# Performance work log

Hardware: AMD Instinct MI355X
Metric: run time of the kernel (lower is better)

Reference implementation:

```python
import jax, jax.numpy as jnp
import numpy as np

NDIM = 1024
NHEAD = 16
HEAD_DIM = NDIM // NHEAD


def setup_inputs() -> dict:
    key = jax.random.key(0)
    ks = jax.random.split(key, 12)
    B, L, C = 2, 2048, NDIM
    s = 0.02
    return {
        "q": jax.random.normal(ks[0], (B, L, C), jnp.float32),
        "k": jax.random.normal(ks[1], (B, L, C), jnp.float32),
        "v": jax.random.normal(ks[2], (B, L, C), jnp.float32),
        "Wq": jax.random.normal(ks[3], (C, C), jnp.float32) * s,
        "bq": jax.random.normal(ks[4], (C,), jnp.float32) * s,
        "Wk": jax.random.normal(ks[5], (C, C), jnp.float32) * s,
        "bk": jax.random.normal(ks[6], (C,), jnp.float32) * s,
        "Wv": jax.random.normal(ks[7], (C, C), jnp.float32) * s,
        "bv": jax.random.normal(ks[8], (C,), jnp.float32) * s,
        "Wo": jax.random.normal(ks[9], (C, C), jnp.float32) * s,
        "bo": jax.random.normal(ks[10], (C,), jnp.float32) * s,
    }


def reference(q, k, v, Wq, bq, Wk, bk, Wv, bv, Wo, bo):
    B, Lq, C = q.shape
    H, D = NHEAD, HEAD_DIM
    # projections, then split heads: (B, H, L, D)
    qh = (q @ Wq + bq).reshape(B, Lq, H, D).transpose(0, 2, 1, 3)
    kh = (k @ Wk + bk).reshape(B, k.shape[1], H, D).transpose(0, 2, 1, 3)
    vh = (v @ Wv + bv).reshape(B, v.shape[1], H, D).transpose(0, 2, 1, 3)
    scale = 1.0 / jnp.sqrt(jnp.asarray(D, qh.dtype))
    att = jnp.einsum("bhqd,bhkd->bhqk", qh, kh) * scale  # (B,H,Lq,Lk)
    att = jax.nn.softmax(att, axis=-1)  # dropout p=0.0 -> identity
    y = jnp.einsum("bhqk,bhkd->bhqd", att, vh)
    y = y.transpose(0, 2, 1, 3).reshape(B, Lq, C)
    return y @ Wo + bo
```

## Files before the change

kernel.cpp:

```cpp
#include <hip/hip_runtime.h>
#include <math.h>

#define BATCH 2
#define SEQ   2048
#define CDIM  1024
#define NHEAD 16
#define HDIM  64
#define TOKS  (BATCH * SEQ)

typedef __bf16 bf16x8 __attribute__((ext_vector_type(8)));
typedef float  f32x4  __attribute__((ext_vector_type(4)));

#define MFMA16(a, b, c) __builtin_amdgcn_mfma_f32_16x16x32_bf16(a, b, c, 0, 0, 0)

#define QSCALE 0.1803368801111204f

__device__ __forceinline__ void gload_lds16(const __bf16* g, __bf16* l) {
    __builtin_amdgcn_global_load_lds(
        (const __attribute__((address_space(1))) unsigned int*)g,
        (__attribute__((address_space(3))) unsigned int*)l, 16, 0, 0);
}

__global__ __launch_bounds__(256) void prep_kernel(
    const float* __restrict__ q, const float* __restrict__ k, const float* __restrict__ v,
    __bf16* __restrict__ qo, __bf16* __restrict__ ko, __bf16* __restrict__ vo,
    const float* __restrict__ W0, const float* __restrict__ W1,
    const float* __restrict__ W2, const float* __restrict__ W3,
    __bf16* __restrict__ T0, __bf16* __restrict__ T1,
    __bf16* __restrict__ T2, __bf16* __restrict__ T3)
{
    __shared__ __bf16 Ts[64][72];
    const int bx = blockIdx.x;
    const int tid = threadIdx.x;

    if (bx < 6144) {
        const int t = bx >> 11;
        const size_t i = ((size_t)(bx & 2047) * 256 + tid) * 8;
        const float* s = t == 0 ? q : (t == 1 ? k : v);
        __bf16* d = t == 0 ? qo : (t == 1 ? ko : vo);
        const float4 x = *(const float4*)&s[i];
        const float4 y = *(const float4*)&s[i + 4];
        bf16x8 o;
        o[0] = (__bf16)x.x; o[1] = (__bf16)x.y; o[2] = (__bf16)x.z; o[3] = (__bf16)x.w;
        o[4] = (__bf16)y.x; o[5] = (__bf16)y.y; o[6] = (__bf16)y.z; o[7] = (__bf16)y.w;
        *(bf16x8*)&d[i] = o;
        return;
    }

    const int t  = bx - 6144;
    const int z  = t >> 8;
    const int ry = (t & 255) >> 4;
    const int rx = t & 15;
    const float* W = z == 0 ? W0 : z == 1 ? W1 : z == 2 ? W2 : W3;
    __bf16* T = z == 0 ? T0 : z == 1 ? T1 : z == 2 ? T2 : T3;
    const int rb = ry * 64, cb = rx * 64;
    const int r = tid >> 4;
    const int c4 = (tid & 15) * 4;
#pragma unroll
    for (int p = 0; p < 4; p++) {
        const int rr = p * 16 + r;
        const float4 w4 = *(const float4*)&W[(size_t)(rb + rr) * CDIM + cb + c4];
        Ts[c4 + 0][rr] = (__bf16)w4.x;
        Ts[c4 + 1][rr] = (__bf16)w4.y;
        Ts[c4 + 2][rr] = (__bf16)w4.z;
        Ts[c4 + 3][rr] = (__bf16)w4.w;
    }
    __syncthreads();
    const int n = tid >> 2;
    const int k16 = (tid & 3) * 16;
    *(bf16x8*)&T[(size_t)(cb + n) * CDIM + rb + k16]     = *(const bf16x8*)&Ts[n][k16];
    *(bf16x8*)&T[(size_t)(cb + n) * CDIM + rb + k16 + 8] = *(const bf16x8*)&Ts[n][k16 + 8];
}

__global__ __launch_bounds__(256) void qkv_gemm_kernel(
    const __bf16* __restrict__ qb, const __bf16* __restrict__ kb,
    const __bf16* __restrict__ vb,
    const __bf16* __restrict__ Wqt, const __bf16* __restrict__ Wkt,
    const __bf16* __restrict__ Wvt,
    const float* __restrict__ bq, const float* __restrict__ bk,
    const float* __restrict__ bv,
    __bf16* __restrict__ Qh, __bf16* __restrict__ Kh, __bf16* __restrict__ Vht)
{
    __shared__ __bf16 As[128 * 32];
    __shared__ __bf16 Bs[128 * 32];

    const int z = blockIdx.z;
    const __bf16* A    = z == 0 ? qb : z == 1 ? kb : Wvt;
    const __bf16* Bt   = z == 0 ? Wqt : z == 1 ? Wkt : vb;
    const float*  bias = z == 0 ? bq : z == 1 ? bk : bv;

    const int tid  = threadIdx.x;
    const int w    = tid >> 6;
    const int lane = tid & 63;
    const int quad = lane >> 4;
    const int c    = lane & 15;
    const int wm   = w >> 1;
    const int wn   = w & 1;
    const int rowBase = (z == 2 ? blockIdx.x : blockIdx.y) * 128;
    const int colBase = (z == 2 ? blockIdx.y : blockIdx.x) * 128;

    const int sr = lane >> 2;
    const int sk = (lane & 3) * 8;

    f32x4 acc[4][4];
#pragma unroll
    for (int i = 0; i < 4; i++)
#pragma unroll
        for (int j = 0; j < 4; j++) acc[i][j] = (f32x4){0, 0, 0, 0};

    for (int k0 = 0; k0 < CDIM; k0 += 32) {
#pragma unroll
        for (int j = 0; j < 2; j++) {
            const int r0 = (w * 2 + j) * 16;
            gload_lds16(A  + (size_t)(rowBase + r0 + sr) * CDIM + k0 + sk, &As[r0 * 32]);
            gload_lds16(Bt + (size_t)(colBase + r0 + sr) * CDIM + k0 + sk, &Bs[r0 * 32]);
        }
        __syncthreads();

        bf16x8 af[4], bf[4];
#pragma unroll
        for (int i = 0; i < 4; i++) {
            af[i] = *(const bf16x8*)&As[(wm * 64 + i * 16 + c) * 32 + quad * 8];
            bf[i] = *(const bf16x8*)&Bs[(wn * 64 + i * 16 + c) * 32 + quad * 8];
        }
#pragma unroll
        for (int mi = 0; mi < 4; mi++)
#pragma unroll
            for (int ni = 0; ni < 4; ni++)
                acc[mi][ni] = MFMA16(af[mi], bf[ni], acc[mi][ni]);
        __syncthreads();
    }

#pragma unroll
    for (int mi = 0; mi < 4; mi++) {
#pragma unroll
        for (int ni = 0; ni < 4; ni++) {
            const int col = colBase + wn * 64 + ni * 16 + c;
#pragma unroll
            for (int r = 0; r < 4; r++) {
                const int row = rowBase + wm * 64 + mi * 16 + quad * 4 + r;
                const float val = acc[mi][ni][r];
                if (z == 2) {
                    Vht[(size_t)row * TOKS + col] = (__bf16)(val + bias[row]);
                } else {
                    const int b = row >> 11, l = row & 2047;
                    const int h = col >> 6,  d = col & 63;
                    const float s = (z == 0) ? QSCALE : 1.0f;
                    __bf16* outp = (z == 0) ? Qh : Kh;
                    outp[((((size_t)b * NHEAD + h) * SEQ) + l) * HDIM + d] =
                        (__bf16)((val + bias[col]) * s);
                }
            }
        }
    }
}

__global__ __launch_bounds__(256) void out_gemm_kernel(
    const __bf16* __restrict__ A, const __bf16* __restrict__ Bt,
    const float* __restrict__ bias, float* __restrict__ out)
{
    __shared__ __bf16 As[128 * 32];
    __shared__ __bf16 Bs[128 * 32];

    const int tid  = threadIdx.x;
    const int w    = tid >> 6;
    const int lane = tid & 63;
    const int quad = lane >> 4;
    const int c    = lane & 15;
    const int wm   = w >> 1;
    const int wn   = w & 1;
    const int rowBase = blockIdx.y * 128;
    const int colBase = blockIdx.x * 128;
    const int sr = lane >> 2;
    const int sk = (lane & 3) * 8;

    f32x4 acc[4][4];
#pragma unroll
    for (int i = 0; i < 4; i++)
#pragma unroll
        for (int j = 0; j < 4; j++) acc[i][j] = (f32x4){0, 0, 0, 0};

    for (int k0 = 0; k0 < CDIM; k0 += 32) {
#pragma unroll
        for (int j = 0; j < 2; j++) {
            const int r0 = (w * 2 + j) * 16;
            gload_lds16(A  + (size_t)(rowBase + r0 + sr) * CDIM + k0 + sk, &As[r0 * 32]);
            gload_lds16(Bt + (size_t)(colBase + r0 + sr) * CDIM + k0 + sk, &Bs[r0 * 32]);
        }
        __syncthreads();

        bf16x8 af[4], bf[4];
#pragma unroll
        for (int i = 0; i < 4; i++) {
            af[i] = *(const bf16x8*)&As[(wm * 64 + i * 16 + c) * 32 + quad * 8];
            bf[i] = *(const bf16x8*)&Bs[(wn * 64 + i * 16 + c) * 32 + quad * 8];
        }
#pragma unroll
        for (int mi = 0; mi < 4; mi++)
#pragma unroll
            for (int ni = 0; ni < 4; ni++)
                acc[mi][ni] = MFMA16(af[mi], bf[ni], acc[mi][ni]);
        __syncthreads();
    }

#pragma unroll
    for (int mi = 0; mi < 4; mi++) {
#pragma unroll
        for (int ni = 0; ni < 4; ni++) {
            const int col = colBase + wn * 64 + ni * 16 + c;
#pragma unroll
            for (int r = 0; r < 4; r++) {
                const int row = rowBase + wm * 64 + mi * 16 + quad * 4 + r;
                out[(size_t)row * CDIM + col] = acc[mi][ni][r] + bias[col];
            }
        }
    }
}

__global__ __launch_bounds__(256) void attn_mfma_kernel(
    const __bf16* __restrict__ Qh, const __bf16* __restrict__ Kh,
    const __bf16* __restrict__ Vht, __bf16* __restrict__ Y)
{
    __shared__ __align__(16) __bf16 Ks[32][72];
    __shared__ __align__(16) __bf16 Vt[64][48];
    __shared__ __align__(16) __bf16 Pf[4][32][48];

    const int tid  = threadIdx.x;
    const int w    = tid >> 6;
    const int lane = tid & 63;
    const int quad = lane >> 4;
    const int c    = lane & 15;
    const int bh   = blockIdx.x;
    const int b    = bh >> 4;
    const int h    = bh & 15;
    const int qbase = blockIdx.y * 128 + w * 32;

    const __bf16* Qg = Qh + (size_t)bh * SEQ * HDIM;
    const __bf16* Kg = Kh + (size_t)bh * SEQ * HDIM;
    const __bf16* Vg = Vht + (size_t)(h * HDIM) * TOKS + (size_t)b * SEQ;

    bf16x8 qf[2][2];
#pragma unroll
    for (int g = 0; g < 2; g++) {
        qf[g][0] = *(const bf16x8*)&Qg[(size_t)(qbase + g * 16 + c) * HDIM + quad * 8];
        qf[g][1] = *(const bf16x8*)&Qg[(size_t)(qbase + g * 16 + c) * HDIM + 32 + quad * 8];
    }

    bf16x8 ones;
#pragma unroll
    for (int j = 0; j < 8; j++) ones[j] = (__bf16)1.0f;

    f32x4 O[2][4];
    f32x4 L[2];
#pragma unroll
    for (int g = 0; g < 2; g++) {
        L[g] = (f32x4){0, 0, 0, 0};
#pragma unroll
        for (int i = 0; i < 4; i++) O[g][i] = (f32x4){0, 0, 0, 0};
    }

    const int skey = tid >> 3, sc8 = (tid & 7) * 8;
    const int sd   = tid >> 2, sk8 = (tid & 3) * 8;

    for (int t0 = 0; t0 < SEQ; t0 += 32) {
        __syncthreads();
        *(bf16x8*)&Ks[skey][sc8] = *(const bf16x8*)&Kg[(size_t)(t0 + skey) * HDIM + sc8];
        *(bf16x8*)&Vt[sd][sk8]   = *(const bf16x8*)&Vg[(size_t)sd * TOKS + t0 + sk8];
        __syncthreads();

        const bf16x8 k00 = *(const bf16x8*)&Ks[c][quad * 8];
        const bf16x8 k01 = *(const bf16x8*)&Ks[c][32 + quad * 8];
        const bf16x8 k10 = *(const bf16x8*)&Ks[16 + c][quad * 8];
        const bf16x8 k11 = *(const bf16x8*)&Ks[16 + c][32 + quad * 8];

#pragma unroll
        for (int g = 0; g < 2; g++) {
            f32x4 s0 = {0, 0, 0, 0}, s1 = {0, 0, 0, 0};
            s0 = MFMA16(qf[g][0], k00, s0);
            s0 = MFMA16(qf[g][1], k01, s0);
            s1 = MFMA16(qf[g][0], k10, s1);
            s1 = MFMA16(qf[g][1], k11, s1);
#pragma unroll
            for (int r = 0; r < 4; r++) {
                Pf[w][g * 16 + quad * 4 + r][c]      = (__bf16)__builtin_amdgcn_exp2f(s0[r]);
                Pf[w][g * 16 + quad * 4 + r][16 + c] = (__bf16)__builtin_amdgcn_exp2f(s1[r]);
            }
        }

        const bf16x8 v0 = *(const bf16x8*)&Vt[c][quad * 8];
        const bf16x8 v1 = *(const bf16x8*)&Vt[16 + c][quad * 8];
        const bf16x8 v2 = *(const bf16x8*)&Vt[32 + c][quad * 8];
        const bf16x8 v3 = *(const bf16x8*)&Vt[48 + c][quad * 8];

#pragma unroll
        for (int g = 0; g < 2; g++) {
            const bf16x8 pf = *(const bf16x8*)&Pf[w][g * 16 + c][quad * 8];
            L[g]    = MFMA16(pf, ones, L[g]);
            O[g][0] = MFMA16(pf, v0, O[g][0]);
            O[g][1] = MFMA16(pf, v1, O[g][1]);
            O[g][2] = MFMA16(pf, v2, O[g][2]);
            O[g][3] = MFMA16(pf, v3, O[g][3]);
        }
    }

    __bf16* Yb = Y + (size_t)b * SEQ * CDIM;
#pragma unroll
    for (int g = 0; g < 2; g++) {
#pragma unroll
        for (int r = 0; r < 4; r++) {
            const float inv = 1.0f / L[g][r];
            const int l = qbase + g * 16 + quad * 4 + r;
            __bf16* yp = Yb + (size_t)l * CDIM + h * HDIM + c;
            yp[0]  = (__bf16)(O[g][0][r] * inv);
            yp[16] = (__bf16)(O[g][1][r] * inv);
            yp[32] = (__bf16)(O[g][2][r] * inv);
            yp[48] = (__bf16)(O[g][3][r] * inv);
        }
    }
}


extern "C" void kernel_launch(void* const* d_in, const int* in_sizes, int n_in,
                              void* d_out, int out_size, void* d_ws, size_t ws_size,
                              hipStream_t stream)
{
    const float* q  = (const float*)d_in[0];
    const float* k  = (const float*)d_in[1];
    const float* v  = (const float*)d_in[2];
    const float* Wq = (const float*)d_in[3];
    const float* bq = (const float*)d_in[4];
    const float* Wk = (const float*)d_in[5];
    const float* bk = (const float*)d_in[6];
    const float* Wv = (const float*)d_in[7];
    const float* bv = (const float*)d_in[8];
    const float* Wo = (const float*)d_in[9];
    const float* bo = (const float*)d_in[10];
    float* out = (float*)d_out;

    const size_t MAT = (size_t)TOKS * CDIM;
    const size_t WN  = (size_t)CDIM * CDIM;

    __bf16* p   = (__bf16*)d_ws;
    __bf16* qb  = p; p += MAT;
    __bf16* kb  = p; p += MAT;
    __bf16* vb  = p; p += MAT;
    __bf16* Wqt = p; p += WN;
    __bf16* Wkt = p; p += WN;
    __bf16* Wvt = p; p += WN;
    __bf16* Wot = p; p += WN;
    __bf16* Qh  = p; p += MAT;
    __bf16* Kh  = p; p += MAT;
    __bf16* Vht = p; p += MAT;
    __bf16* Yb  = qb;

    const dim3 blk(256);

    prep_kernel<<<dim3(6144 + 1024), blk, 0, stream>>>(
        q, k, v, qb, kb, vb, Wq, Wk, Wv, Wo, Wqt, Wkt, Wvt, Wot);

    qkv_gemm_kernel<<<dim3(8, 32, 3), blk, 0, stream>>>(
        qb, kb, vb, Wqt, Wkt, Wvt, bq, bk, bv, Qh, Kh, Vht);

    attn_mfma_kernel<<<dim3(BATCH * NHEAD, SEQ / 128), blk, 0, stream>>>(Qh, Kh, Vht, Yb);

    out_gemm_kernel<<<dim3(8, 32), blk, 0, stream>>>(Yb, Wot, bo, out);
}
```

Baseline: 248.0 us.

## Rewrite attention as single-wave register-pipelined kernel; permute V layout; narrow output tiles

The attention kernel now runs one wave per block over 64 queries. K and V fragments are loaded straight from global memory into double-buffered registers, replacing the LDS staging and block barriers. V is stored with a permuted column order so the P fragments can be written to LDS as packed bf16 pairs. The output GEMM tile drops from 128x128 to 128x64 to launch more blocks. The cost is more register pressure and uncoalesced global loads in attention, plus less data reuse per block in the output GEMM.

After: 262.7 us. 1.06x slower.

```diff
diff --git a/kernel.cpp b/kernel.cpp
--- a/kernel.cpp
+++ b/kernel.cpp
@@ -9,6 +9,7 @@
 #define TOKS  (BATCH * SEQ)
 
 typedef __bf16 bf16x8 __attribute__((ext_vector_type(8)));
+typedef __bf16 bf16x2 __attribute__((ext_vector_type(2)));
 typedef float  f32x4  __attribute__((ext_vector_type(4)));
 
 #define MFMA16(a, b, c) __builtin_amdgcn_mfma_f32_16x16x32_bf16(a, b, c, 0, 0, 0)
@@ -141,7 +142,8 @@
                 const int row = rowBase + wm * 64 + mi * 16 + quad * 4 + r;
                 const float val = acc[mi][ni][r];
                 if (z == 2) {
-                    Vht[(size_t)row * TOKS + col] = (__bf16)(val + bias[row]);
+                    const int col2 = (col & ~31) | (((col & 15) << 1) | ((col >> 4) & 1));
+                    Vht[(size_t)row * TOKS + col2] = (__bf16)(val + bias[row]);
                 } else {
                     const int b = row >> 11, l = row & 2047;
                     const int h = col >> 6,  d = col & 63;
@@ -160,7 +162,7 @@
     const float* __restrict__ bias, float* __restrict__ out)
 {
     __shared__ __bf16 As[128 * 32];
-    __shared__ __bf16 Bs[128 * 32];
+    __shared__ __bf16 Bs[64 * 32];
 
     const int tid  = threadIdx.x;
     const int w    = tid >> 6;
@@ -170,35 +172,36 @@
     const int wm   = w >> 1;
     const int wn   = w & 1;
     const int rowBase = blockIdx.y * 128;
-    const int colBase = blockIdx.x * 128;
+    const int colBase = blockIdx.x * 64;
     const int sr = lane >> 2;
     const int sk = (lane & 3) * 8;
 
-    f32x4 acc[4][4];
+    f32x4 acc[4][2];
 #pragma unroll
     for (int i = 0; i < 4; i++)
 #pragma unroll
-        for (int j = 0; j < 4; j++) acc[i][j] = (f32x4){0, 0, 0, 0};
+        for (int j = 0; j < 2; j++) acc[i][j] = (f32x4){0, 0, 0, 0};
 
     for (int k0 = 0; k0 < CDIM; k0 += 32) {
 #pragma unroll
         for (int j = 0; j < 2; j++) {
             const int r0 = (w * 2 + j) * 16;
-            gload_lds16(A  + (size_t)(rowBase + r0 + sr) * CDIM + k0 + sk, &As[r0 * 32]);
-            gload_lds16(Bt + (size_t)(colBase + r0 + sr) * CDIM + k0 + sk, &Bs[r0 * 32]);
-        }
+            gload_lds16(A + (size_t)(rowBase + r0 + sr) * CDIM + k0 + sk, &As[r0 * 32]);
+        }
+        gload_lds16(Bt + (size_t)(colBase + w * 16 + sr) * CDIM + k0 + sk, &Bs[w * 16 * 32]);
         __syncthreads();
 
-        bf16x8 af[4], bf[4];
-#pragma unroll
-        for (int i = 0; i < 4; i++) {
+        bf16x8 af[4], bf[2];
+#pragma unroll
+        for (int i = 0; i < 4; i++)
             af[i] = *(const bf16x8*)&As[(wm * 64 + i * 16 + c) * 32 + quad * 8];
-            bf[i] = *(const bf16x8*)&Bs[(wn * 64 + i * 16 + c) * 32 + quad * 8];
-        }
+#pragma unroll
+        for (int i = 0; i < 2; i++)
+            bf[i] = *(const bf16x8*)&Bs[(wn * 32 + i * 16 + c) * 32 + quad * 8];
 #pragma unroll
         for (int mi = 0; mi < 4; mi++)
 #pragma unroll
-            for (int ni = 0; ni < 4; ni++)
+            for (int ni = 0; ni < 2; ni++)
                 acc[mi][ni] = MFMA16(af[mi], bf[ni], acc[mi][ni]);
         __syncthreads();
     }
@@ -206,8 +209,8 @@
 #pragma unroll
     for (int mi = 0; mi < 4; mi++) {
 #pragma unroll
-        for (int ni = 0; ni < 4; ni++) {
-            const int col = colBase + wn * 64 + ni * 16 + c;
+        for (int ni = 0; ni < 2; ni++) {
+            const int col = colBase + wn * 32 + ni * 16 + c;
 #pragma unroll
             for (int r = 0; r < 4; r++) {
                 const int row = rowBase + wm * 64 + mi * 16 + quad * 4 + r;
@@ -217,31 +220,33 @@
     }
 }
 
-__global__ __launch_bounds__(256) void attn_mfma_kernel(
+struct AttnRegs {
+    bf16x8 k[4];
+    bf16x8 v[4];
+};
+
+__global__ __launch_bounds__(64) void attn_v3_kernel(
     const __bf16* __restrict__ Qh, const __bf16* __restrict__ Kh,
     const __bf16* __restrict__ Vht, __bf16* __restrict__ Y)
 {
-    __shared__ __align__(16) __bf16 Ks[32][72];
-    __shared__ __align__(16) __bf16 Vt[64][48];
-    __shared__ __align__(16) __bf16 Pf[4][32][48];
-
-    const int tid  = threadIdx.x;
-    const int w    = tid >> 6;
-    const int lane = tid & 63;
+    __shared__ unsigned int Pf[4][16][36];
+
+    const int lane = threadIdx.x;
     const int quad = lane >> 4;
     const int c    = lane & 15;
-    const int bh   = blockIdx.x;
+    const int qt   = blockIdx.x;
+    const int bh   = blockIdx.y;
     const int b    = bh >> 4;
     const int h    = bh & 15;
-    const int qbase = blockIdx.y * 128 + w * 32;
+    const int qbase = qt * 64;
 
     const __bf16* Qg = Qh + (size_t)bh * SEQ * HDIM;
     const __bf16* Kg = Kh + (size_t)bh * SEQ * HDIM;
     const __bf16* Vg = Vht + (size_t)(h * HDIM) * TOKS + (size_t)b * SEQ;
 
-    bf16x8 qf[2][2];
-#pragma unroll
-    for (int g = 0; g < 2; g++) {
+    bf16x8 qf[4][2];
+#pragma unroll
+    for (int g = 0; g < 4; g++) {
         qf[g][0] = *(const bf16x8*)&Qg[(size_t)(qbase + g * 16 + c) * HDIM + quad * 8];
         qf[g][1] = *(const bf16x8*)&Qg[(size_t)(qbase + g * 16 + c) * HDIM + 32 + quad * 8];
     }
@@ -250,62 +255,70 @@
 #pragma unroll
     for (int j = 0; j < 8; j++) ones[j] = (__bf16)1.0f;
 
-    f32x4 O[2][4];
-    f32x4 L[2];
-#pragma unroll
-    for (int g = 0; g < 2; g++) {
+    f32x4 O[4][4];
+    f32x4 L[4];
+#pragma unroll
+    for (int g = 0; g < 4; g++) {
         L[g] = (f32x4){0, 0, 0, 0};
 #pragma unroll
         for (int i = 0; i < 4; i++) O[g][i] = (f32x4){0, 0, 0, 0};
     }
 
-    const int skey = tid >> 3, sc8 = (tid & 7) * 8;
-    const int sd   = tid >> 2, sk8 = (tid & 3) * 8;
-
-    for (int t0 = 0; t0 < SEQ; t0 += 32) {
-        __syncthreads();
-        *(bf16x8*)&Ks[skey][sc8] = *(const bf16x8*)&Kg[(size_t)(t0 + skey) * HDIM + sc8];
-        *(bf16x8*)&Vt[sd][sk8]   = *(const bf16x8*)&Vg[(size_t)sd * TOKS + t0 + sk8];
-        __syncthreads();
-
-        const bf16x8 k00 = *(const bf16x8*)&Ks[c][quad * 8];
-        const bf16x8 k01 = *(const bf16x8*)&Ks[c][32 + quad * 8];
-        const bf16x8 k10 = *(const bf16x8*)&Ks[16 + c][quad * 8];
-        const bf16x8 k11 = *(const bf16x8*)&Ks[16 + c][32 + quad * 8];
-
-#pragma unroll
-        for (int g = 0; g < 2; g++) {
+    AttnRegs ra, rb;
+
+    const size_t kOff0 = (size_t)c * HDIM + quad * 8;
+    const size_t kOff1 = kOff0 + 32;
+    const size_t kOff2 = (size_t)(16 + c) * HDIM + quad * 8;
+    const size_t kOff3 = kOff2 + 32;
+
+    auto load_tile = [&](AttnRegs& r, int t) {
+        r.k[0] = *(const bf16x8*)&Kg[(size_t)t * HDIM + kOff0];
+        r.k[1] = *(const bf16x8*)&Kg[(size_t)t * HDIM + kOff1];
+        r.k[2] = *(const bf16x8*)&Kg[(size_t)t * HDIM + kOff2];
+        r.k[3] = *(const bf16x8*)&Kg[(size_t)t * HDIM + kOff3];
+#pragma unroll
+        for (int i = 0; i < 4; i++)
+            r.v[i] = *(const bf16x8*)&Vg[(size_t)(c + 16 * i) * TOKS + t + quad * 8];
+    };
+
+    auto step = [&](const AttnRegs& cur) {
+#pragma unroll
+        for (int g = 0; g < 4; g++) {
             f32x4 s0 = {0, 0, 0, 0}, s1 = {0, 0, 0, 0};
-            s0 = MFMA16(qf[g][0], k00, s0);
-            s0 = MFMA16(qf[g][1], k01, s0);
-            s1 = MFMA16(qf[g][0], k10, s1);
-            s1 = MFMA16(qf[g][1], k11, s1);
+            s0 = MFMA16(qf[g][0], cur.k[0], s0);
+            s0 = MFMA16(qf[g][1], cur.k[1], s0);
+            s1 = MFMA16(qf[g][0], cur.k[2], s1);
+            s1 = MFMA16(qf[g][1], cur.k[3], s1);
 #pragma unroll
             for (int r = 0; r < 4; r++) {
-                Pf[w][g * 16 + quad * 4 + r][c]      = (__bf16)__builtin_amdgcn_exp2f(s0[r]);
-                Pf[w][g * 16 + quad * 4 + r][16 + c] = (__bf16)__builtin_amdgcn_exp2f(s1[r]);
+                union { bf16x2 v; unsigned int u; } pk;
+                pk.v[0] = (__bf16)__builtin_amdgcn_exp2f(s0[r]);
+                pk.v[1] = (__bf16)__builtin_amdgcn_exp2f(s1[r]);
+                Pf[g][quad * 4 + r][c] = pk.u;
             }
         }
-
-        const bf16x8 v0 = *(const bf16x8*)&Vt[c][quad * 8];
-        const bf16x8 v1 = *(const bf16x8*)&Vt[16 + c][quad * 8];
-        const bf16x8 v2 = *(const bf16x8*)&Vt[32 + c][quad * 8];
-        const bf16x8 v3 = *(const bf16x8*)&Vt[48 + c][quad * 8];
-
-#pragma unroll
-        for (int g = 0; g < 2; g++) {
-            const bf16x8 pf = *(const bf16x8*)&Pf[w][g * 16 + c][quad * 8];
+#pragma unroll
+        for (int g = 0; g < 4; g++) {
+            const bf16x8 pf = *(const bf16x8*)&Pf[g][c][quad * 4];
             L[g]    = MFMA16(pf, ones, L[g]);
-            O[g][0] = MFMA16(pf, v0, O[g][0]);
-            O[g][1] = MFMA16(pf, v1, O[g][1]);
-            O[g][2] = MFMA16(pf, v2, O[g][2]);
-            O[g][3] = MFMA16(pf, v3, O[g][3]);
-        }
+            O[g][0] = MFMA16(pf, cur.v[0], O[g][0]);
+            O[g][1] = MFMA16(pf, cur.v[1], O[g][1]);
+            O[g][2] = MFMA16(pf, cur.v[2], O[g][2]);
+            O[g][3] = MFMA16(pf, cur.v[3], O[g][3]);
+        }
+    };
+
+    load_tile(ra, 0);
+    for (int t0 = 0; t0 < SEQ; t0 += 64) {
+        load_tile(rb, (t0 + 32) & (SEQ - 1));
+        step(ra);
+        load_tile(ra, (t0 + 64) & (SEQ - 1));
+        step(rb);
     }
 
     __bf16* Yb = Y + (size_t)b * SEQ * CDIM;
 #pragma unroll
-    for (int g = 0; g < 2; g++) {
+    for (int g = 0; g < 4; g++) {
 #pragma unroll
         for (int r = 0; r < 4; r++) {
             const float inv = 1.0f / L[g][r];
@@ -353,15 +366,13 @@
     __bf16* Vht = p; p += MAT;
     __bf16* Yb  = qb;
 
-    const dim3 blk(256);
-
-    prep_kernel<<<dim3(6144 + 1024), blk, 0, stream>>>(
+    prep_kernel<<<dim3(7168), dim3(256), 0, stream>>>(
         q, k, v, qb, kb, vb, Wq, Wk, Wv, Wo, Wqt, Wkt, Wvt, Wot);
 
-    qkv_gemm_kernel<<<dim3(8, 32, 3), blk, 0, stream>>>(
+    qkv_gemm_kernel<<<dim3(8, 32, 3), dim3(256), 0, stream>>>(
         qb, kb, vb, Wqt, Wkt, Wvt, bq, bk, bv, Qh, Kh, Vht);
 
-    attn_mfma_kernel<<<dim3(BATCH * NHEAD, SEQ / 128), blk, 0, stream>>>(Qh, Kh, Vht, Yb);
-
-    out_gemm_kernel<<<dim3(8, 32), blk, 0, stream>>>(Yb, Wot, bo, out);
-}
+    attn_v3_kernel<<<dim3(32, 32), dim3(64), 0, stream>>>(Qh, Kh, Vht, Yb);
+
+    out_gemm_kernel<<<dim3(16, 32), dim3(256), 0, stream>>>(Yb, Wot, bo, out);
+}
```
